# Performance work log

Measured on AMD Instinct MI355X. Metric: run time of the kernel, lower is better.

## Reference

```python
import jax, jax.numpy as jnp
import numpy as np


def setup_inputs() -> dict:
    key = jax.random.key(0)
    ks = jax.random.split(key, 6)
    B, T, S, D, H, V = 8, 256, 512, 768, 8, 32000
    return {
        "dec_output": jax.random.normal(ks[0], (B, T, D), dtype=jnp.float32),
        "final_output": jax.random.normal(ks[1], (B, T, V), dtype=jnp.float32),
        "attention_weights": jax.random.normal(ks[2], (B, H, T, S), dtype=jnp.float32),
        "encoder_input": jax.random.randint(ks[3], (B, S), 0, V, dtype=jnp.int32),
        "W": jax.random.normal(ks[4], (D, 1), dtype=jnp.float32) * 0.02,
        "b": jnp.zeros((1,), dtype=jnp.float32),
        "inp_shape": S,
        "tar_shape": T,
        "batch": B,
        "training": 0,
    }


def reference(dec_output, final_output, attention_weights, encoder_input, W, b,
              inp_shape, tar_shape, batch, training):
    B, T, V = final_output.shape
    # p_gen: Dense(1, sigmoid) on decoder output -> [B, T, 1]
    p_gen = jax.nn.sigmoid(jnp.einsum("btd,do->bto", dec_output, W) + b)
    # vocab distribution scaled by p_gen
    vocab_dist = p_gen * jax.nn.softmax(final_output, axis=-1)  # [B, T, V]
    # mean over heads, softmax over source positions -> [B, T, S]
    attention_dist = jax.nn.softmax(jnp.mean(attention_weights, axis=1), axis=-1)
    updates = (1.0 - p_gen) * attention_dist  # [B, T, S]
    # scatter-add attention mass onto source token ids in vocab space
    b_idx = jnp.arange(B)[:, None, None]           # [B,1,1]
    t_idx = jnp.arange(T)[None, :, None]           # [1,T,1]
    v_idx = encoder_input[:, None, :]              # [B,1,S]
    copy_probs = jnp.zeros((B, T, V), dtype=vocab_dist.dtype).at[
        b_idx, t_idx, v_idx].add(updates)
    combined_logits = jnp.log(vocab_dist + copy_probs + 0.001)
    return combined_logits
```

## Files before the change

kernel.cpp:

```cpp
#include <hip/hip_runtime.h>
#include <stdint.h>

#define B_ 8
#define T_ 256
#define S_ 512
#define D_ 768
#define H_ 8
#define V_ 32000
#define BLOCK 1024
#define NWAVE (BLOCK / 64)
#define NF4 (V_ / 4)

typedef float vf4 __attribute__((ext_vector_type(4)));

static __device__ __forceinline__ float h2f(unsigned short u) {
    _Float16 h = __builtin_bit_cast(_Float16, u);
    return (float)h;
}
static __device__ __forceinline__ unsigned short f2h(float f) {
    _Float16 h = (_Float16)f;
    return __builtin_bit_cast(unsigned short, h);
}

static __device__ __forceinline__ void lds_atomic_add_f16(unsigned short* arr, int idx, float val) {
    unsigned int* word = (unsigned int*)arr + (idx >> 1);
    const bool hi = (idx & 1) != 0;
    unsigned int old = *word, assumed;
    do {
        assumed = old;
        unsigned short bits = hi ? (unsigned short)(assumed >> 16)
                                 : (unsigned short)(assumed & 0xFFFFu);
        unsigned short nb = f2h(h2f(bits) + val);
        unsigned int nw = hi ? ((assumed & 0x0000FFFFu) | ((unsigned int)nb << 16))
                             : ((assumed & 0xFFFF0000u) | (unsigned int)nb);
        old = atomicCAS(word, assumed, nw);
    } while (old != assumed);
}

static __device__ __forceinline__ vf4 expv(vf4 v) {
    vf4 r;
    r.x = __expf(v.x);
    r.y = __expf(v.y);
    r.z = __expf(v.z);
    r.w = __expf(v.w);
    return r;
}
static __device__ __forceinline__ float sum4(vf4 v) {
    return v.x + v.y + v.z + v.w;
}

__global__ __launch_bounds__(BLOCK, 8) void ptrgen_f32(
    const float* __restrict__ dec,
    const float* __restrict__ fin,
    const float* __restrict__ attw,
    const int* __restrict__ enc,
    const float* __restrict__ W,
    const float* __restrict__ bbias,
    float* __restrict__ out)
{
    __shared__ __align__(16) unsigned short copyp[V_];
    __shared__ float sred[3 * NWAVE];
    __shared__ float sbc[3];

    const int tid = threadIdx.x;
    const int bid = blockIdx.x;
    const int b = bid >> 8;
    const int t = bid & 255;

    uint4* cz = (uint4*)copyp;
#pragma unroll
    for (int i = 0; i < 4; ++i) {
        const int idx = tid + i * BLOCK;
        if (idx < V_ / 8) cz[idx] = make_uint4(0u, 0u, 0u, 0u);
    }

    float pp = 0.0f;
    if (tid < D_) pp = dec[(size_t)bid * D_ + tid] * W[tid];

    __syncthreads();

    float aep = 0.0f;
    if (tid < S_) {
        const float* ab = attw + ((size_t)(b * H_) * T_ + t) * S_ + tid;
        float s = 0.0f;
#pragma unroll
        for (int h = 0; h < H_; ++h) s += ab[(size_t)h * (T_ * S_)];
        const float ae = __expf(s * (1.0f / H_));
        aep = ae;
        lds_atomic_add_f16(copyp, enc[b * S_ + tid], ae);
    }

    const vf4* rowf = (const vf4*)(fin + (size_t)bid * V_);
    const bool has7 = tid < (NF4 - 7 * BLOCK);
    const vf4 e0 = expv(__builtin_nontemporal_load(rowf + tid));
    const vf4 e1 = expv(__builtin_nontemporal_load(rowf + tid + 1 * BLOCK));
    const vf4 e2 = expv(__builtin_nontemporal_load(rowf + tid + 2 * BLOCK));
    const vf4 e3 = expv(__builtin_nontemporal_load(rowf + tid + 3 * BLOCK));
    const vf4 e4_ = expv(__builtin_nontemporal_load(rowf + tid + 4 * BLOCK));
    const vf4 e5 = expv(__builtin_nontemporal_load(rowf + tid + 5 * BLOCK));
    const vf4 e6 = expv(__builtin_nontemporal_load(rowf + tid + 6 * BLOCK));
    vf4 e7 = (vf4)(0.0f);
    if (has7) e7 = expv(__builtin_nontemporal_load(rowf + tid + 7 * BLOCK));
    float lsum = sum4(e0) + sum4(e1) + sum4(e2) + sum4(e3) +
                 sum4(e4_) + sum4(e5) + sum4(e6) + sum4(e7);

    const int lane = tid & 63, wid = tid >> 6;
    float v0 = pp, v1 = aep, v2 = lsum;
#pragma unroll
    for (int o = 32; o; o >>= 1) {
        v0 += __shfl_xor(v0, o, 64);
        v1 += __shfl_xor(v1, o, 64);
        v2 += __shfl_xor(v2, o, 64);
    }
    if (lane == 0) {
        sred[wid] = v0;
        sred[NWAVE + wid] = v1;
        sred[2 * NWAVE + wid] = v2;
    }
    __syncthreads();
    if (wid == 0) {
        float a0 = (lane < NWAVE) ? sred[lane] : 0.0f;
        float a1 = (lane < NWAVE) ? sred[NWAVE + lane] : 0.0f;
        float a2 = (lane < NWAVE) ? sred[2 * NWAVE + lane] : 0.0f;
#pragma unroll
        for (int o = 32; o; o >>= 1) {
            a0 += __shfl_xor(a0, o, 64);
            a1 += __shfl_xor(a1, o, 64);
            a2 += __shfl_xor(a2, o, 64);
        }
        if (lane == 0) { sbc[0] = a0; sbc[1] = a1; sbc[2] = a2; }
    }
    __syncthreads();

    const float p_gen  = 1.0f / (1.0f + __expf(-(sbc[0] + bbias[0])));
    const float inv_l  = p_gen / sbc[2];
    const float cscale = (1.0f - p_gen) / sbc[1];

    vf4* outp = (vf4*)(out + (size_t)bid * V_);
    const uint2* cp2 = (const uint2*)copyp;

    auto emit = [&](int c, vf4 e, uint2 cp) {
        vf4 y;
        y.x = __logf(fmaf(e.x, inv_l,
                          fmaf(h2f((unsigned short)(cp.x & 0xFFFFu)), cscale, 0.001f)));
        y.y = __logf(fmaf(e.y, inv_l,
                          fmaf(h2f((unsigned short)(cp.x >> 16)), cscale, 0.001f)));
        y.z = __logf(fmaf(e.z, inv_l,
                          fmaf(h2f((unsigned short)(cp.y & 0xFFFFu)), cscale, 0.001f)));
        y.w = __logf(fmaf(e.w, inv_l,
                          fmaf(h2f((unsigned short)(cp.y >> 16)), cscale, 0.001f)));
        __builtin_nontemporal_store(y, outp + c);
    };

    emit(tid,             e0,  cp2[tid]);
    emit(tid + 1 * BLOCK, e1,  cp2[tid + 1 * BLOCK]);
    emit(tid + 2 * BLOCK, e2,  cp2[tid + 2 * BLOCK]);
    emit(tid + 3 * BLOCK, e3,  cp2[tid + 3 * BLOCK]);
    emit(tid + 4 * BLOCK, e4_, cp2[tid + 4 * BLOCK]);
    emit(tid + 5 * BLOCK, e5,  cp2[tid + 5 * BLOCK]);
    emit(tid + 6 * BLOCK, e6,  cp2[tid + 6 * BLOCK]);
    if (has7) emit(tid + 7 * BLOCK, e7, cp2[tid + 7 * BLOCK]);
}

extern "C" void kernel_launch(void* const* d_in, const int* in_sizes, int n_in,
                              void* d_out, int out_size, void* d_ws, size_t ws_size,
                              hipStream_t stream) {
    const float* dec   = (const float*)d_in[0];
    const float* fin   = (const float*)d_in[1];
    const float* attw  = (const float*)d_in[2];
    const int*   enc   = (const int*)d_in[3];
    const float* W     = (const float*)d_in[4];
    const float* bbias = (const float*)d_in[5];
    float* out = (float*)d_out;

    ptrgen_f32<<<B_ * T_, BLOCK, 0, stream>>>(dec, fin, attw, enc, W, bbias, out);
}
```

Measured before the change: 454.6 us.

## Replace dense fp16 LDS copy table with sparse hash map and bitmap

Replaces the 32000-entry fp16 LDS scatter table with a 1024-slot open-addressing hash (fp32 values) plus a vocab bitmap. This cuts LDS from about 64KB to about 12KB per block, which should allow more resident blocks, and it also removes the fp16 CAS loop. The block size drops to 512, and each row of final_output is now read twice (once for the softmax sum, once in the emit pass) instead of being held in registers. The extra global read traffic is the main risk, since the kernel is bandwidth bound. The change also restores fp32 accumulation of copy probabilities.

```diff
diff --git a/kernel.cpp b/kernel.cpp
--- a/kernel.cpp
+++ b/kernel.cpp
@@ -7,46 +7,17 @@
 #define D_ 768
 #define H_ 8
 #define V_ 32000
-#define BLOCK 1024
+#define BLOCK 512
 #define NWAVE (BLOCK / 64)
 #define NF4 (V_ / 4)
+#define SLOTS 1024
+#define EMPTYK 0xFFFFFFFFu
+#define BMW ((V_ + 31) / 32)
 
 typedef float vf4 __attribute__((ext_vector_type(4)));
 
-static __device__ __forceinline__ float h2f(unsigned short u) {
-    _Float16 h = __builtin_bit_cast(_Float16, u);
-    return (float)h;
-}
-static __device__ __forceinline__ unsigned short f2h(float f) {
-    _Float16 h = (_Float16)f;
-    return __builtin_bit_cast(unsigned short, h);
-}
-
-static __device__ __forceinline__ void lds_atomic_add_f16(unsigned short* arr, int idx, float val) {
-    unsigned int* word = (unsigned int*)arr + (idx >> 1);
-    const bool hi = (idx & 1) != 0;
-    unsigned int old = *word, assumed;
-    do {
-        assumed = old;
-        unsigned short bits = hi ? (unsigned short)(assumed >> 16)
-                                 : (unsigned short)(assumed & 0xFFFFu);
-        unsigned short nb = f2h(h2f(bits) + val);
-        unsigned int nw = hi ? ((assumed & 0x0000FFFFu) | ((unsigned int)nb << 16))
-                             : ((assumed & 0xFFFF0000u) | (unsigned int)nb);
-        old = atomicCAS(word, assumed, nw);
-    } while (old != assumed);
-}
-
-static __device__ __forceinline__ vf4 expv(vf4 v) {
-    vf4 r;
-    r.x = __expf(v.x);
-    r.y = __expf(v.y);
-    r.z = __expf(v.z);
-    r.w = __expf(v.w);
-    return r;
-}
-static __device__ __forceinline__ float sum4(vf4 v) {
-    return v.x + v.y + v.z + v.w;
+static __device__ __forceinline__ float e4(vf4 v) {
+    return __expf(v.x) + __expf(v.y) + __expf(v.z) + __expf(v.w);
 }
 
 __global__ __launch_bounds__(BLOCK, 8) void ptrgen_f32(
@@ -58,7 +29,9 @@
     const float* __restrict__ bbias,
     float* __restrict__ out)
 {
-    __shared__ __align__(16) unsigned short copyp[V_];
+    __shared__ unsigned int hkey[SLOTS];
+    __shared__ float        hval[SLOTS];
+    __shared__ unsigned int bmap[BMW];
     __shared__ float sred[3 * NWAVE];
     __shared__ float sbc[3];
 
@@ -67,45 +40,45 @@
     const int b = bid >> 8;
     const int t = bid & 255;
 
-    uint4* cz = (uint4*)copyp;
 #pragma unroll
-    for (int i = 0; i < 4; ++i) {
-        const int idx = tid + i * BLOCK;
-        if (idx < V_ / 8) cz[idx] = make_uint4(0u, 0u, 0u, 0u);
-    }
+    for (int i = tid; i < SLOTS; i += BLOCK) { hkey[i] = EMPTYK; hval[i] = 0.0f; }
+    for (int i = tid; i < BMW; i += BLOCK) bmap[i] = 0u;
 
-    float pp = 0.0f;
-    if (tid < D_) pp = dec[(size_t)bid * D_ + tid] * W[tid];
+    float pp = dec[(size_t)bid * D_ + tid] * W[tid];
+    if (tid < D_ - BLOCK)
+        pp += dec[(size_t)bid * D_ + BLOCK + tid] * W[BLOCK + tid];
+
+    const float* ab = attw + ((size_t)(b * H_) * T_ + t) * S_ + tid;
+    float s = 0.0f;
+#pragma unroll
+    for (int h = 0; h < H_; ++h) s += ab[(size_t)h * (T_ * S_)];
+    const float ae = __expf(s * (1.0f / H_));
+    const int token = enc[b * S_ + tid];
 
     __syncthreads();
 
-    float aep = 0.0f;
-    if (tid < S_) {
-        const float* ab = attw + ((size_t)(b * H_) * T_ + t) * S_ + tid;
-        float s = 0.0f;
-#pragma unroll
-        for (int h = 0; h < H_; ++h) s += ab[(size_t)h * (T_ * S_)];
-        const float ae = __expf(s * (1.0f / H_));
-        aep = ae;
-        lds_atomic_add_f16(copyp, enc[b * S_ + tid], ae);
+    atomicOr(&bmap[token >> 5], 1u << (token & 31));
+    {
+        unsigned int h = ((unsigned int)token * 2654435761u) >> 22;
+        for (;;) {
+            unsigned int prev = atomicCAS(&hkey[h], EMPTYK, (unsigned int)token);
+            if (prev == EMPTYK || prev == (unsigned int)token) {
+                atomicAdd(&hval[h], ae);
+                break;
+            }
+            h = (h + 1) & (SLOTS - 1);
+        }
     }
 
     const vf4* rowf = (const vf4*)(fin + (size_t)bid * V_);
-    const bool has7 = tid < (NF4 - 7 * BLOCK);
-    const vf4 e0 = expv(__builtin_nontemporal_load(rowf + tid));
-    const vf4 e1 = expv(__builtin_nontemporal_load(rowf + tid + 1 * BLOCK));
-    const vf4 e2 = expv(__builtin_nontemporal_load(rowf + tid + 2 * BLOCK));
-    const vf4 e3 = expv(__builtin_nontemporal_load(rowf + tid + 3 * BLOCK));
-    const vf4 e4_ = expv(__builtin_nontemporal_load(rowf + tid + 4 * BLOCK));
-    const vf4 e5 = expv(__builtin_nontemporal_load(rowf + tid + 5 * BLOCK));
-    const vf4 e6 = expv(__builtin_nontemporal_load(rowf + tid + 6 * BLOCK));
-    vf4 e7 = (vf4)(0.0f);
-    if (has7) e7 = expv(__builtin_nontemporal_load(rowf + tid + 7 * BLOCK));
-    float lsum = sum4(e0) + sum4(e1) + sum4(e2) + sum4(e3) +
-                 sum4(e4_) + sum4(e5) + sum4(e6) + sum4(e7);
+    float lsum = 0.0f;
+#pragma unroll 5
+    for (int i = 0; i < 15; ++i) lsum += e4(rowf[tid + i * BLOCK]);
+    if (tid < NF4 - 15 * BLOCK)
+        lsum += e4(rowf[tid + 15 * BLOCK]);
 
     const int lane = tid & 63, wid = tid >> 6;
-    float v0 = pp, v1 = aep, v2 = lsum;
+    float v0 = pp, v1 = ae, v2 = lsum;
 #pragma unroll
     for (int o = 32; o; o >>= 1) {
         v0 += __shfl_xor(v0, o, 64);
@@ -123,7 +96,7 @@
         float a1 = (lane < NWAVE) ? sred[NWAVE + lane] : 0.0f;
         float a2 = (lane < NWAVE) ? sred[2 * NWAVE + lane] : 0.0f;
 #pragma unroll
-        for (int o = 32; o; o >>= 1) {
+        for (int o = 4; o; o >>= 1) {
             a0 += __shfl_xor(a0, o, 64);
             a1 += __shfl_xor(a1, o, 64);
             a2 += __shfl_xor(a2, o, 64);
@@ -137,29 +110,35 @@
     const float cscale = (1.0f - p_gen) / sbc[1];
 
     vf4* outp = (vf4*)(out + (size_t)bid * V_);
-    const uint2* cp2 = (const uint2*)copyp;
 
-    auto emit = [&](int c, vf4 e, uint2 cp) {
-        vf4 y;
-        y.x = __logf(fmaf(e.x, inv_l,
-                          fmaf(h2f((unsigned short)(cp.x & 0xFFFFu)), cscale, 0.001f)));
-        y.y = __logf(fmaf(e.y, inv_l,
-                          fmaf(h2f((unsigned short)(cp.x >> 16)), cscale, 0.001f)));
-        y.z = __logf(fmaf(e.z, inv_l,
-                          fmaf(h2f((unsigned short)(cp.y & 0xFFFFu)), cscale, 0.001f)));
-        y.w = __logf(fmaf(e.w, inv_l,
-                          fmaf(h2f((unsigned short)(cp.y >> 16)), cscale, 0.001f)));
-        __builtin_nontemporal_store(y, outp + c);
+    auto hget = [&](int idx) -> float {
+        unsigned int h = ((unsigned int)idx * 2654435761u) >> 22;
+        for (;;) {
+            unsigned int k = hkey[h];
+            if (k == (unsigned int)idx) return hval[h];
+            if (k == EMPTYK) return 0.0f;
+            h = (h + 1) & (SLOTS - 1);
+        }
     };
 
-    emit(tid,             e0,  cp2[tid]);
-    emit(tid + 1 * BLOCK, e1,  cp2[tid + 1 * BLOCK]);
-    emit(tid + 2 * BLOCK, e2,  cp2[tid + 2 * BLOCK]);
-    emit(tid + 3 * BLOCK, e3,  cp2[tid + 3 * BLOCK]);
-    emit(tid + 4 * BLOCK, e4_, cp2[tid + 4 * BLOCK]);
-    emit(tid + 5 * BLOCK, e5,  cp2[tid + 5 * BLOCK]);
-    emit(tid + 6 * BLOCK, e6,  cp2[tid + 6 * BLOCK]);
-    if (has7) emit(tid + 7 * BLOCK, e7, cp2[tid + 7 * BLOCK]);
+#pragma unroll 4
+    for (int c = tid; c < NF4; c += BLOCK) {
+        const vf4 x = __builtin_nontemporal_load(rowf + c);
+        const unsigned int nib = (bmap[c >> 3] >> ((c & 7) * 4)) & 0xFu;
+        float c0 = 0.0f, c1 = 0.0f, c2 = 0.0f, c3 = 0.0f;
+        if (nib) {
+            if (nib & 1u) c0 = hget(4 * c + 0);
+            if (nib & 2u) c1 = hget(4 * c + 1);
+            if (nib & 4u) c2 = hget(4 * c + 2);
+            if (nib & 8u) c3 = hget(4 * c + 3);
+        }
+        vf4 y;
+        y.x = __logf(fmaf(__expf(x.x), inv_l, fmaf(c0, cscale, 0.001f)));
+        y.y = __logf(fmaf(__expf(x.y), inv_l, fmaf(c1, cscale, 0.001f)));
+        y.z = __logf(fmaf(__expf(x.z), inv_l, fmaf(c2, cscale, 0.001f)));
+        y.w = __logf(fmaf(__expf(x.w), inv_l, fmaf(c3, cscale, 0.001f)));
+        __builtin_nontemporal_store(y, outp + c);
+    }
 }
 
 extern "C" void kernel_launch(void* const* d_in, const int* in_sizes, int n_in,
```

Result: slower. 492.3 us (+8.3%).
